# Optimization experiments

Measured on AMD Instinct MI355X. Metric: run time of the kernel, lower is better.

The kernel has to match this reference:

```python
import jax, jax.numpy as jnp
import numpy as np

B, S, D = 2, 2048, 1024
H, DH = 16, 64
DM = 4096
NEG = 1e10


def setup_inputs() -> dict:
    key = jax.random.key(0)
    ks = jax.random.split(key, 8)
    sc = 1.0 / np.sqrt(D)
    return {
        "x": jax.random.normal(ks[0], (B, S, D), jnp.float32),
        "W_Q": jax.random.normal(ks[1], (H, DH, D), jnp.float32) * sc,
        "W_K": jax.random.normal(ks[2], (H, DH, D), jnp.float32) * sc,
        "W_V": jax.random.normal(ks[3], (H, DH, D), jnp.float32) * sc,
        "W_O": jax.random.normal(ks[4], (D, H * DH), jnp.float32) * sc,
        "W_in": jax.random.normal(ks[5], (DM, D), jnp.float32) * sc,
        "b_in": jnp.zeros((DM,), jnp.float32),
        "W_out": jax.random.normal(ks[6], (D, DM), jnp.float32) * sc,
        "b_out": jnp.zeros((D,), jnp.float32),
    }


def reference(x, W_Q, W_K, W_V, W_O, W_in, b_in, W_out, b_out):
    b, s, d = x.shape
    d_head = W_Q.shape[1]
    # --- Attention (faithful to original einsum/mask formulation) ---
    q = jnp.einsum('ihd,bpd->biph', W_Q, x)
    k = jnp.einsum('ihd,bpd->biph', W_K, x)
    v = jnp.einsum('ihd,bpd->biph', W_V, x)
    scores = jnp.einsum('biph,biqh->biqp', k, q)  # [b,i,q,p]
    # original: t.tril(scores) - 1e10 * (1 - triu(ones)) ; mask buffer is triu
    triu = jnp.triu(jnp.ones((s, s), x.dtype))
    masked = jnp.tril(scores) - NEG * (1.0 - triu)
    attn = jax.nn.softmax(masked / np.sqrt(d_head), axis=-1)
    z = jnp.einsum('biph,biqp->biqh', v, attn)          # [b,i,q,h]
    z_flat = z.transpose(0, 2, 1, 3).reshape(b, s, -1)   # b q (i h)
    attn_out = jnp.einsum('df,bqf->bqd', W_O, z_flat)
    # --- Block residual structure (as written: x = attn(x); x = x + x) ---
    mid = attn_out + attn_out
    # --- MLP ---
    pre = jnp.einsum('md,bpd->bpm', W_in, mid) + b_in
    h = jax.nn.relu(pre)
    mlp_out = jnp.einsum('dm,bpm->bpd', W_out, h) + b_out
    return mid + mlp_out
```

## Files before the change

kernel.cpp:

```cpp
#include <hip/hip_runtime.h>
#include <hip/hip_bf16.h>
#include <stdint.h>

typedef unsigned short ushort_t;
typedef __attribute__((ext_vector_type(8))) short short8;
typedef __attribute__((ext_vector_type(4))) float floatx4;

#define DEV __device__ __forceinline__

DEV ushort_t f2b(float f) {
  uint32_t x = __float_as_uint(f);
  uint32_t r = (x + 0x7FFFu + ((x >> 16) & 1u)) >> 16;
  return (ushort_t)r;
}
DEV float b2f(ushort_t u) { return __uint_as_float(((uint32_t)u) << 16); }

DEV void async16(const ushort_t* g, ushort_t* l) {
  __builtin_amdgcn_global_load_lds(
      (const __attribute__((address_space(1))) void*)g,
      (__attribute__((address_space(3))) void*)l, 16, 0, 0);
}

struct Cvt7 {
  const float* src[7];
  ushort_t* dst[7];
  unsigned start[8];
};
__global__ void cvt_all(Cvt7 a) {
  unsigned idx = blockIdx.x * blockDim.x + threadIdx.x;
  if (idx >= a.start[7]) return;
  int seg = 0;
#pragma unroll
  for (int j = 1; j < 7; j++) seg += (idx >= a.start[j]) ? 1 : 0;
  unsigned off = idx - a.start[seg];
  float4 v = ((const float4*)a.src[seg])[off];
  ((ushort4*)a.dst[seg])[off] = make_ushort4(f2b(v.x), f2b(v.y), f2b(v.z), f2b(v.w));
}

template <int MODE>
__launch_bounds__(256)
__global__ void gemm_bt(const ushort_t* __restrict__ A, const ushort_t* __restrict__ Bm,
                        int M, int N, int K,
                        ushort_t* __restrict__ outB, float* __restrict__ outF,
                        const float* __restrict__ bias) {
  __shared__ alignas(16) ushort_t As[128 * 64];
  __shared__ alignas(16) ushort_t Bs[128 * 64];
  const int tid = threadIdx.x;
  const int wave = tid >> 6, lane = tid & 63;
  const int wm = wave >> 1, wn = wave & 1;
  const int m0 = blockIdx.y * 128, n0 = blockIdx.x * 128;

  floatx4 acc[4][4];
#pragma unroll
  for (int i = 0; i < 4; i++)
#pragma unroll
    for (int j = 0; j < 4; j++) acc[i][j] = (floatx4){0.f, 0.f, 0.f, 0.f};

  const int srow = wave * 32 + (lane >> 3);
  const int scol = (((lane & 7) ^ ((lane >> 3) & 7)) * 8);
  const ushort_t* gA = A + (size_t)(m0 + srow) * K + scol;
  const ushort_t* gB = Bm + (size_t)(n0 + srow) * K + scol;
  ushort_t* lA = As + wave * 2048;
  ushort_t* lB = Bs + wave * 2048;

  const int fr = lane & 15, fq = lane >> 4;
  const ushort_t* rdA = As + (wm * 64 + fr) * 64;
  const ushort_t* rdB = Bs + (wn * 64 + fr) * 64;
  const int sw = fr & 7;

  for (int k0 = 0; k0 < K; k0 += 64) {
#pragma unroll
    for (int j = 0; j < 4; j++) {
      async16(gA + (size_t)j * 8 * K, lA + j * 512);
      async16(gB + (size_t)j * 8 * K, lB + j * 512);
    }
    gA += 64; gB += 64;
    __syncthreads();
#pragma unroll
    for (int h = 0; h < 2; h++) {
      const int co = ((h * 4 + fq) ^ sw) * 8;
      short8 af[4], bfv[4];
#pragma unroll
      for (int mt = 0; mt < 4; mt++) af[mt] = *(const short8*)(rdA + mt * 16 * 64 + co);
#pragma unroll
      for (int nt = 0; nt < 4; nt++) bfv[nt] = *(const short8*)(rdB + nt * 16 * 64 + co);
#pragma unroll
      for (int mt = 0; mt < 4; mt++)
#pragma unroll
        for (int nt = 0; nt < 4; nt++)
          acc[mt][nt] = __builtin_amdgcn_mfma_f32_16x16x32_bf16(af[mt], bfv[nt], acc[mt][nt], 0, 0, 0);
    }
    __syncthreads();
  }

  const int crow = m0 + wm * 64 + (lane >> 4) * 4;
  const int ccol = n0 + wn * 64 + (lane & 15);
#pragma unroll
  for (int mt = 0; mt < 4; mt++)
#pragma unroll
    for (int nt = 0; nt < 4; nt++) {
      floatx4 a = acc[mt][nt];
#pragma unroll
      for (int r = 0; r < 4; r++) {
        const int gm = crow + mt * 16 + r;
        const int gn = ccol + nt * 16;
        const size_t idx = (size_t)gm * N + gn;
        float v = a[r];
        if constexpr (MODE == 0) {
          outB[idx] = f2b(v);
        } else if constexpr (MODE == 1) {
          float t = 2.f * v;
          outB[idx] = f2b(t);
          outF[idx] = t + bias[gn];
        } else if constexpr (MODE == 2) {
          float t = v + bias[gn];
          outB[idx] = f2b(t > 0.f ? t : 0.f);
        } else {
          outF[idx] += v;
        }
      }
    }
}

__launch_bounds__(256)
__global__ void attn1(const ushort_t* __restrict__ qkv,
                      float* __restrict__ eG, float* __restrict__ psumG) {
  const int c = blockIdx.x & 31;
  const int i = (blockIdx.x >> 5) & 15;
  const int b = blockIdx.x >> 9;
  const int t = threadIdx.x, wave = t >> 6, h = t & 63;
  const size_t rowbase = (size_t)b * 2048 * 3072;
  float vacc = 0.f;
#pragma unroll 4
  for (int r = 0; r < 16; r++) {
    const int s = c * 64 + wave * 16 + r;
    const size_t rb = rowbase + (size_t)s * 3072 + i * 64 + h;
    float q = b2f(qkv[rb]);
    float k = b2f(qkv[rb + 1024]);
    float v = b2f(qkv[rb + 2048]);
    float d = q * k;
#pragma unroll
    for (int off = 32; off > 0; off >>= 1) d += __shfl_xor(d, off, 64);
    if (h == 0) eG[((size_t)(b * 16 + i)) * 2048 + s] = __expf(d * 0.125f);
    vacc += v;
  }
  __shared__ float vs[4][64];
  vs[wave][h] = vacc;
  __syncthreads();
  if (t < 64)
    psumG[(((size_t)(b * 16 + i)) * 32 + c) * 64 + t] =
        vs[0][t] + vs[1][t] + vs[2][t] + vs[3][t];
}

__launch_bounds__(256)
__global__ void attn2(const ushort_t* __restrict__ qkv,
                      const float* __restrict__ eG, const float* __restrict__ psumG,
                      ushort_t* __restrict__ Z) {
  const int wave = threadIdx.x >> 6, h = threadIdx.x & 63;
  const int c = (blockIdx.x & 7) * 4 + wave;
  const int i = (blockIdx.x >> 3) & 15;
  const int b = blockIdx.x >> 7;
  const size_t rowbase = (size_t)b * 2048 * 3072;
  const size_t pbase = ((size_t)(b * 16 + i)) * 32;
  float run = 0.f;
#pragma unroll 8
  for (int cc = c + 1; cc < 32; cc++) run += psumG[(pbase + cc) * 64 + h];
  const size_t ebase = ((size_t)(b * 16 + i)) * 2048;
  for (int t4 = 3; t4 >= 0; t4--) {
    float vv[16], ee[16];
#pragma unroll
    for (int j = 0; j < 16; j++) {
      const int s = c * 64 + t4 * 16 + j;
      vv[j] = b2f(qkv[rowbase + (size_t)s * 3072 + 2048 + i * 64 + h]);
      ee[j] = eG[ebase + s];
    }
#pragma unroll
    for (int j = 15; j >= 0; j--) {
      const int s = c * 64 + t4 * 16 + j;
      float z = (ee[j] * vv[j] + run) / (ee[j] + (float)(2047 - s));
      Z[((size_t)b * 2048 + s) * 1024 + i * 64 + h] = f2b(z);
      run += vv[j];
    }
  }
}

extern "C" void kernel_launch(void* const* d_in, const int* in_sizes, int n_in,
                              void* d_out, int out_size, void* d_ws, size_t ws_size,
                              hipStream_t stream) {
  const float* x     = (const float*)d_in[0];
  const float* W_Q   = (const float*)d_in[1];
  const float* W_K   = (const float*)d_in[2];
  const float* W_V   = (const float*)d_in[3];
  const float* W_O   = (const float*)d_in[4];
  const float* W_in  = (const float*)d_in[5];
  const float* b_in  = (const float*)d_in[6];
  const float* W_out = (const float*)d_in[7];
  const float* b_out = (const float*)d_in[8];
  float* out = (float*)d_out;

  char* base = (char*)d_ws;
  const size_t MB = 1048576;
  ushort_t* Xb    = (ushort_t*)(base + 0 * MB);
  ushort_t* Wqkv  = (ushort_t*)(base + 8 * MB);
  ushort_t* WOb   = (ushort_t*)(base + 14 * MB);
  ushort_t* Z     = (ushort_t*)(base + 16 * MB);
  ushort_t* QKV   = (ushort_t*)(base + 24 * MB);
  ushort_t* midb  = (ushort_t*)(base + 48 * MB);
  ushort_t* Winb  = (ushort_t*)(base + 56 * MB);
  ushort_t* Woutb = (ushort_t*)(base + 64 * MB);
  ushort_t* Hb    = (ushort_t*)(base + 72 * MB);
  float*    eG    = (float*)(base + 104 * MB);
  float*    psumG = (float*)(base + 104 * MB + 262144);

  Cvt7 ca;
  ca.src[0] = x;     ca.dst[0] = Xb;
  ca.src[1] = W_Q;   ca.dst[1] = Wqkv;
  ca.src[2] = W_K;   ca.dst[2] = Wqkv + 1048576;
  ca.src[3] = W_V;   ca.dst[3] = Wqkv + 2097152;
  ca.src[4] = W_O;   ca.dst[4] = WOb;
  ca.src[5] = W_in;  ca.dst[5] = Winb;
  ca.src[6] = W_out; ca.dst[6] = Woutb;
  unsigned n4s[7] = {1048576, 262144, 262144, 262144, 262144, 1048576, 1048576};
  unsigned acc4 = 0;
  for (int j = 0; j < 7; j++) { ca.start[j] = acc4; acc4 += n4s[j]; }
  ca.start[7] = acc4;
  cvt_all<<<dim3((acc4 + 255) / 256), dim3(256), 0, stream>>>(ca);

  gemm_bt<0><<<dim3(24, 32), 256, 0, stream>>>(Xb, Wqkv, 4096, 3072, 1024,
                                               QKV, nullptr, nullptr);
  attn1<<<dim3(1024), 256, 0, stream>>>(QKV, eG, psumG);
  attn2<<<dim3(256), 256, 0, stream>>>(QKV, eG, psumG, Z);
  gemm_bt<1><<<dim3(8, 32), 256, 0, stream>>>(Z, WOb, 4096, 1024, 1024,
                                              midb, out, b_out);
  gemm_bt<2><<<dim3(32, 32), 256, 0, stream>>>(midb, Winb, 4096, 4096, 1024,
                                               Hb, nullptr, b_in);
  gemm_bt<3><<<dim3(8, 32), 256, 0, stream>>>(Hb, Woutb, 4096, 1024, 4096,
                                              nullptr, out, b_out);
}
```

Before: 327.5 us.

## Double-buffer LDS tiles in low-occupancy GEMMs to overlap loads with MFMA

Adds a DBUF template flag to the bf16 GEMM. When it is set, two LDS buffers are used so the async global-to-LDS loads for the next K tile are issued before computing the current one. It is enabled only for the out-projection and down-projection GEMMs, whose 256-block grids leave the GPU underoccupied and so gain little latency hiding from other blocks. The cost is double the LDS per block, 64KB, which can lower occupancy. The other GEMMs keep the single-buffer path.

```diff
diff --git a/kernel.cpp b/kernel.cpp
--- a/kernel.cpp
+++ b/kernel.cpp
@@ -37,14 +37,14 @@
   ((ushort4*)a.dst[seg])[off] = make_ushort4(f2b(v.x), f2b(v.y), f2b(v.z), f2b(v.w));
 }
 
-template <int MODE>
+template <int MODE, bool DBUF>
 __launch_bounds__(256)
 __global__ void gemm_bt(const ushort_t* __restrict__ A, const ushort_t* __restrict__ Bm,
                         int M, int N, int K,
                         ushort_t* __restrict__ outB, float* __restrict__ outF,
                         const float* __restrict__ bias) {
-  __shared__ alignas(16) ushort_t As[128 * 64];
-  __shared__ alignas(16) ushort_t Bs[128 * 64];
+  __shared__ alignas(16) ushort_t As[(DBUF ? 2 : 1) * 128 * 64];
+  __shared__ alignas(16) ushort_t Bs[(DBUF ? 2 : 1) * 128 * 64];
   const int tid = threadIdx.x;
   const int wave = tid >> 6, lane = tid & 63;
   const int wm = wave >> 1, wn = wave & 1;
@@ -60,37 +60,57 @@
   const int scol = (((lane & 7) ^ ((lane >> 3) & 7)) * 8);
   const ushort_t* gA = A + (size_t)(m0 + srow) * K + scol;
   const ushort_t* gB = Bm + (size_t)(n0 + srow) * K + scol;
-  ushort_t* lA = As + wave * 2048;
-  ushort_t* lB = Bs + wave * 2048;
 
   const int fr = lane & 15, fq = lane >> 4;
-  const ushort_t* rdA = As + (wm * 64 + fr) * 64;
-  const ushort_t* rdB = Bs + (wn * 64 + fr) * 64;
   const int sw = fr & 7;
 
-  for (int k0 = 0; k0 < K; k0 += 64) {
+  auto issueAB = [&](int buf) {
+    ushort_t* lA = As + buf * 8192 + wave * 2048;
+    ushort_t* lB = Bs + buf * 8192 + wave * 2048;
 #pragma unroll
     for (int j = 0; j < 4; j++) {
       async16(gA + (size_t)j * 8 * K, lA + j * 512);
       async16(gB + (size_t)j * 8 * K, lB + j * 512);
     }
     gA += 64; gB += 64;
-    __syncthreads();
+  };
+  auto compute = [&](int buf) {
+    const ushort_t* rA = As + buf * 8192 + (wm * 64 + fr) * 64;
+    const ushort_t* rB = Bs + buf * 8192 + (wn * 64 + fr) * 64;
 #pragma unroll
     for (int h = 0; h < 2; h++) {
       const int co = ((h * 4 + fq) ^ sw) * 8;
       short8 af[4], bfv[4];
 #pragma unroll
-      for (int mt = 0; mt < 4; mt++) af[mt] = *(const short8*)(rdA + mt * 16 * 64 + co);
-#pragma unroll
-      for (int nt = 0; nt < 4; nt++) bfv[nt] = *(const short8*)(rdB + nt * 16 * 64 + co);
+      for (int mt = 0; mt < 4; mt++) af[mt] = *(const short8*)(rA + mt * 16 * 64 + co);
+#pragma unroll
+      for (int nt = 0; nt < 4; nt++) bfv[nt] = *(const short8*)(rB + nt * 16 * 64 + co);
 #pragma unroll
       for (int mt = 0; mt < 4; mt++)
 #pragma unroll
         for (int nt = 0; nt < 4; nt++)
           acc[mt][nt] = __builtin_amdgcn_mfma_f32_16x16x32_bf16(af[mt], bfv[nt], acc[mt][nt], 0, 0, 0);
     }
-    __syncthreads();
+  };
+
+  if constexpr (DBUF) {
+    const int nk = K >> 6;
+    issueAB(0);
+    for (int k = 0; k < nk; k += 2) {
+      __syncthreads();
+      issueAB(1);
+      compute(0);
+      __syncthreads();
+      if (k + 2 < nk) issueAB(0);
+      compute(1);
+    }
+  } else {
+    for (int k0 = 0; k0 < K; k0 += 64) {
+      issueAB(0);
+      __syncthreads();
+      compute(0);
+      __syncthreads();
+    }
   }
 
   const int crow = m0 + wm * 64 + (lane >> 4) * 4;
@@ -226,14 +246,14 @@
   ca.start[7] = acc4;
   cvt_all<<<dim3((acc4 + 255) / 256), dim3(256), 0, stream>>>(ca);
 
-  gemm_bt<0><<<dim3(24, 32), 256, 0, stream>>>(Xb, Wqkv, 4096, 3072, 1024,
-                                               QKV, nullptr, nullptr);
+  gemm_bt<0, false><<<dim3(24, 32), 256, 0, stream>>>(Xb, Wqkv, 4096, 3072, 1024,
+                                                      QKV, nullptr, nullptr);
   attn1<<<dim3(1024), 256, 0, stream>>>(QKV, eG, psumG);
   attn2<<<dim3(256), 256, 0, stream>>>(QKV, eG, psumG, Z);
-  gemm_bt<1><<<dim3(8, 32), 256, 0, stream>>>(Z, WOb, 4096, 1024, 1024,
-                                              midb, out, b_out);
-  gemm_bt<2><<<dim3(32, 32), 256, 0, stream>>>(midb, Winb, 4096, 4096, 1024,
-                                               Hb, nullptr, b_in);
-  gemm_bt<3><<<dim3(8, 32), 256, 0, stream>>>(Hb, Woutb, 4096, 1024, 4096,
-                                              nullptr, out, b_out);
-}
+  gemm_bt<1, true><<<dim3(8, 32), 256, 0, stream>>>(Z, WOb, 4096, 1024, 1024,
+                                                    midb, out, b_out);
+  gemm_bt<2, false><<<dim3(32, 32), 256, 0, stream>>>(midb, Winb, 4096, 4096, 1024,
+                                                      Hb, nullptr, b_in);
+  gemm_bt<3, true><<<dim3(8, 32), 256, 0, stream>>>(Hb, Woutb, 4096, 1024, 4096,
+                                                    nullptr, out, b_out);
+}
```

Result: slower. 342.1 us (+4.4%).
